# Optimization experiments

Hardware: AMD Instinct MI355X
Metric: run time of the kernel (lower is better)

Reference implementation:

```python
import jax, jax.numpy as jnp
import numpy as np

N, E, H, D, IN = 50000, 800000, 4, 64, 2  # nodes, edges, heads, head_dim, in_dim
NEG_SLOPE = 0.2  # DGL GATConv default leaky_relu slope


def setup_inputs() -> dict:
    key = jax.random.key(0)
    ks = jax.random.split(key, 16)
    p = lambda k, shape: jax.random.normal(k, shape, jnp.float32) * 0.1
    return dict(
        positions=jax.random.normal(ks[0], (N, IN), jnp.float32),
        src=jax.random.randint(ks[1], (E,), 0, N, jnp.int32),
        dst=jax.random.randint(ks[2], (E,), 0, N, jnp.int32),
        # conv1: in=2 -> 4 heads x 64; residual needs a projection (2 != 256)
        W1=p(ks[3], (IN, H * D)), al1=p(ks[4], (H, D)), ar1=p(ks[5], (H, D)),
        resW1=p(ks[6], (IN, H * D)),
        # conv2/conv3: in=256 == H*D -> identity residual in DGL
        W2=p(ks[7], (H * D, H * D)), al2=p(ks[8], (H, D)), ar2=p(ks[9], (H, D)),
        W3=p(ks[10], (H * D, H * D)), al3=p(ks[11], (H, D)), ar3=p(ks[12], (H, D)),
        # edge-scoring MLP: Linear(64,64)+ReLU, Linear(64,1)+Sigmoid
        mW1=p(ks[13], (D, D)), mb1=jnp.zeros((D,), jnp.float32),
        mW2=p(ks[14], (D, 1)), mb2=jnp.zeros((1,), jnp.float32),
    )


def _gat_layer(h, W, al, ar, src, dst, res, activation):
    """One DGL-style GATConv. h:[N,Fin] -> [N,H,D]. res:[N,H,D] residual."""
    feat = (h @ W).reshape(N, H, D)
    el = (feat * al).sum(-1)                       # [N,H]
    er = (feat * ar).sum(-1)                       # [N,H]
    e = jax.nn.leaky_relu(el[src] + er[dst], NEG_SLOPE)  # [E,H]
    # edge softmax over incoming edges of each dst node
    emax = jax.ops.segment_max(e, dst, num_segments=N)
    emax = jnp.where(jnp.isfinite(emax), emax, 0.0)      # guard empty segments
    ex = jnp.exp(e - emax[dst])
    den = jax.ops.segment_sum(ex, dst, num_segments=N)
    alpha = ex / jnp.maximum(den, 1e-9)[dst]             # [E,H]
    out = jax.ops.segment_sum(feat[src] * alpha[:, :, None], dst, num_segments=N)
    out = out + res
    if activation:
        out = jax.nn.relu(out)
    return out


def reference(positions, W1, al1, ar1, resW1, W2, al2, ar2, W3, al3, ar3,
              mW1, mb1, mW2, mb2, src, dst):
    res1 = (positions @ resW1).reshape(N, H, D)
    h = _gat_layer(positions, W1, al1, ar1, src, dst, res1, True).reshape(N, H * D)
    h = _gat_layer(h, W2, al2, ar2, src, dst, h.reshape(N, H, D), True).reshape(N, H * D)
    h = _gat_layer(h, W3, al3, ar3, src, dst, h.reshape(N, H, D), False).mean(1)  # [N,D]
    x = jnp.abs(h[src] - h[dst])                   # [E,D]
    score = jax.nn.sigmoid(jax.nn.relu(x @ mW1 + mb1) @ mW2 + mb2)
    return score.squeeze(-1)                       # [E]
```

## Files before the change

kernel.cpp:

```cpp
#include <hip/hip_runtime.h>
#include <hip/hip_bf16.h>

#define NN 50000
#define EE 800000

typedef short short8 __attribute__((ext_vector_type(8)));
typedef float f32x4 __attribute__((ext_vector_type(4)));

__device__ __forceinline__ float lrelu(float x) { return x > 0.f ? x : 0.2f * x; }

__device__ __forceinline__ unsigned short f2bf(float x) {
    __hip_bfloat16 b = __float2bfloat16(x);
    return *(unsigned short*)&b;
}
__device__ __forceinline__ float bf2f(unsigned short u) {
    return __uint_as_float(((unsigned int)u) << 16);
}

__global__ void hist_k(const int* __restrict__ dst, int* __restrict__ deg) {
    int i = blockIdx.x * 256 + threadIdx.x;
    if (i < EE) atomicAdd(&deg[dst[i]], 1);
}

__global__ __launch_bounds__(1024) void scan_k(const int* __restrict__ deg,
                                               int* __restrict__ row_ptr,
                                               int* __restrict__ cursor) {
    __shared__ int wsum[16];
    int tid = threadIdx.x, lane = tid & 63, w = tid >> 6;
    int carry = 0;
    for (int base = 0; base < NN; base += 1024) {
        int i = base + tid;
        int v = (i < NN) ? deg[i] : 0;
        int x = v;
#pragma unroll
        for (int off = 1; off < 64; off <<= 1) {
            int y = __shfl_up(x, off);
            if (lane >= off) x += y;
        }
        if (lane == 63) wsum[w] = x;
        __syncthreads();
        if (tid < 16) {
            int s = wsum[tid];
#pragma unroll
            for (int off = 1; off < 16; off <<= 1) {
                int y = __shfl_up(s, off);
                if (tid >= off) s += y;
            }
            wsum[tid] = s;
        }
        __syncthreads();
        int woff = w ? wsum[w - 1] : 0;
        int excl = carry + woff + x - v;
        if (i < NN) { row_ptr[i] = excl; cursor[i] = excl; }
        carry += wsum[15];
        __syncthreads();
    }
    if (tid == 0) row_ptr[NN] = carry;
}

__global__ void scatter_k(const int* __restrict__ src, const int* __restrict__ dst,
                          int* __restrict__ cursor, int* __restrict__ csr_src) {
    int i = blockIdx.x * 256 + threadIdx.x;
    if (i < EE) {
        int slot = atomicAdd(&cursor[dst[i]], 1);
        csr_src[slot] = src[i];
    }
}

__global__ __launch_bounds__(256) void bconv_k(const float* __restrict__ W2,
                                               const float* __restrict__ W3,
                                               const float* __restrict__ mW1,
                                               unsigned short* __restrict__ BT2,
                                               unsigned short* __restrict__ BT3,
                                               unsigned short* __restrict__ W1Tb) {
    int tid = blockIdx.x * 256 + threadIdx.x;
    int k = tid & 255, n = tid >> 8;
    BT2[n * 256 + k] = f2bf(W2[k * 256 + n]);
    BT3[n * 256 + k] = f2bf(W3[k * 256 + n]);
    if (tid < 4096) {
        int kk = tid & 63, nn = tid >> 6;
        W1Tb[nn * 64 + kk] = f2bf(mW1[kk * 64 + nn]);
    }
}

__global__ __launch_bounds__(256) void eler1_k(const float* __restrict__ pos,
                                               const float* __restrict__ W1,
                                               const float* __restrict__ al,
                                               const float* __restrict__ ar,
                                               float* __restrict__ el,
                                               float* __restrict__ er) {
    int wid = blockIdx.x * 4 + (threadIdx.x >> 6);
    int lane = threadIdx.x & 63;
    if (wid >= NN) return;
    int f = lane * 4;
    float4 w0 = *(const float4*)&W1[f];
    float4 w1 = *(const float4*)&W1[256 + f];
    float4 a4 = *(const float4*)&al[f];
    float4 r4 = *(const float4*)&ar[f];
    float2 p = *(const float2*)&pos[wid * 2];
    float fx = p.x * w0.x + p.y * w1.x;
    float fy = p.x * w0.y + p.y * w1.y;
    float fz = p.x * w0.z + p.y * w1.z;
    float fw = p.x * w0.w + p.y * w1.w;
    float pl = fx * a4.x + fy * a4.y + fz * a4.z + fw * a4.w;
    float pr = fx * r4.x + fy * r4.y + fz * r4.z + fw * r4.w;
#pragma unroll
    for (int off = 1; off < 16; off <<= 1) {
        pl += __shfl_xor(pl, off);
        pr += __shfl_xor(pr, off);
    }
    if ((lane & 15) == 0) {
        int h = lane >> 4;
        el[wid * 4 + h] = pl;
        er[wid * 4 + h] = pr;
    }
}

__global__ __launch_bounds__(256) void eler_b_k(const unsigned short* __restrict__ featb,
                                                const float* __restrict__ al,
                                                const float* __restrict__ ar,
                                                float* __restrict__ el,
                                                float* __restrict__ er) {
    int wid = blockIdx.x * 4 + (threadIdx.x >> 6);
    int lane = threadIdx.x & 63;
    if (wid >= NN) return;
    int f = lane * 4;
    ushort4 u = *(const ushort4*)&featb[(size_t)wid * 256 + f];
    float4 a4 = *(const float4*)&al[f];
    float4 r4 = *(const float4*)&ar[f];
    float vx = bf2f(u.x), vy = bf2f(u.y), vz = bf2f(u.z), vw = bf2f(u.w);
    float pl = vx * a4.x + vy * a4.y + vz * a4.z + vw * a4.w;
    float pr = vx * r4.x + vy * r4.y + vz * r4.z + vw * r4.w;
#pragma unroll
    for (int off = 1; off < 16; off <<= 1) {
        pl += __shfl_xor(pl, off);
        pr += __shfl_xor(pr, off);
    }
    if ((lane & 15) == 0) {
        int h = lane >> 4;
        el[wid * 4 + h] = pl;
        er[wid * 4 + h] = pr;
    }
}

__global__ __launch_bounds__(256) void agg1_k(const float* __restrict__ pos,
                                              const float* __restrict__ W1,
                                              const float* __restrict__ resW1,
                                              const float* __restrict__ el,
                                              const float* __restrict__ er,
                                              const int* __restrict__ row_ptr,
                                              const int* __restrict__ csr_src,
                                              float* __restrict__ hout,
                                              unsigned short* __restrict__ hb16) {
    int wid = blockIdx.x * 4 + (threadIdx.x >> 6);
    int lane = threadIdx.x & 63;
    if (wid >= NN) return;
    int f = lane * 4;
    int start = row_ptr[wid], end = row_ptr[wid + 1];
    int h = lane >> 4;
    float eh = er[wid * 4 + h];

    float ap0 = 0.f, ap1 = 0.f, den = 0.f;
    int s = start;
    for (; s + 3 < end; s += 4) {
        int sn0 = csr_src[s], sn1 = csr_src[s + 1];
        int sn2 = csr_src[s + 2], sn3 = csr_src[s + 3];
        float e0 = el[sn0 * 4 + h], e1 = el[sn1 * 4 + h];
        float e2 = el[sn2 * 4 + h], e3 = el[sn3 * 4 + h];
        float2 p0 = *(const float2*)&pos[sn0 * 2];
        float2 p1 = *(const float2*)&pos[sn1 * 2];
        float2 p2 = *(const float2*)&pos[sn2 * 2];
        float2 p3 = *(const float2*)&pos[sn3 * 2];
        float w0 = __expf(lrelu(e0 + eh)), w1 = __expf(lrelu(e1 + eh));
        float w2 = __expf(lrelu(e2 + eh)), w3 = __expf(lrelu(e3 + eh));
        den += (w0 + w1) + (w2 + w3);
        ap0 += w0 * p0.x + w1 * p1.x + w2 * p2.x + w3 * p3.x;
        ap1 += w0 * p0.y + w1 * p1.y + w2 * p2.y + w3 * p3.y;
    }
    for (; s < end; ++s) {
        int sn = csr_src[s];
        float w = __expf(lrelu(el[sn * 4 + h] + eh));
        float2 p = *(const float2*)&pos[sn * 2];
        den += w;
        ap0 += w * p.x;
        ap1 += w * p.y;
    }
    float inv = 1.f / fmaxf(den, 1e-9f);
    ap0 *= inv;
    ap1 *= inv;

    float4 w0 = *(const float4*)&W1[f];
    float4 w1 = *(const float4*)&W1[256 + f];
    float4 rw0 = *(const float4*)&resW1[f];
    float4 rw1 = *(const float4*)&resW1[256 + f];
    float2 pd = *(const float2*)&pos[wid * 2];
    float4 o;
    o.x = fmaxf(ap0 * w0.x + ap1 * w1.x + pd.x * rw0.x + pd.y * rw1.x, 0.f);
    o.y = fmaxf(ap0 * w0.y + ap1 * w1.y + pd.x * rw0.y + pd.y * rw1.y, 0.f);
    o.z = fmaxf(ap0 * w0.z + ap1 * w1.z + pd.x * rw0.z + pd.y * rw1.z, 0.f);
    o.w = fmaxf(ap0 * w0.w + ap1 * w1.w + pd.x * rw0.w + pd.y * rw1.w, 0.f);
    *(float4*)&hout[(size_t)wid * 256 + f] = o;
    ushort4 ob;
    ob.x = f2bf(o.x); ob.y = f2bf(o.y); ob.z = f2bf(o.z); ob.w = f2bf(o.w);
    *(ushort4*)&hb16[(size_t)wid * 256 + f] = ob;
}

__global__ __launch_bounds__(256) void agg_k(const unsigned short* __restrict__ featb,
                                             const float* __restrict__ el,
                                             const float* __restrict__ er,
                                             const int* __restrict__ row_ptr,
                                             const int* __restrict__ csr_src,
                                             float* __restrict__ hio,
                                             unsigned short* __restrict__ hb16) {
    int wid = blockIdx.x * 4 + (threadIdx.x >> 6);
    int lane = threadIdx.x & 63;
    if (wid >= NN) return;
    int f = lane * 4;
    int start = row_ptr[wid], end = row_ptr[wid + 1];
    int h = lane >> 4;
    float eh = er[wid * 4 + h];

    float4 acc = {0.f, 0.f, 0.f, 0.f};
    float den = 0.f;
    int s = start;
    for (; s + 3 < end; s += 4) {
        int sn0 = csr_src[s], sn1 = csr_src[s + 1];
        int sn2 = csr_src[s + 2], sn3 = csr_src[s + 3];
        float e0 = el[sn0 * 4 + h], e1 = el[sn1 * 4 + h];
        float e2 = el[sn2 * 4 + h], e3 = el[sn3 * 4 + h];
        ushort4 v0 = *(const ushort4*)&featb[(size_t)sn0 * 256 + f];
        ushort4 v1 = *(const ushort4*)&featb[(size_t)sn1 * 256 + f];
        ushort4 v2 = *(const ushort4*)&featb[(size_t)sn2 * 256 + f];
        ushort4 v3 = *(const ushort4*)&featb[(size_t)sn3 * 256 + f];
        float w0 = __expf(lrelu(e0 + eh)), w1 = __expf(lrelu(e1 + eh));
        float w2 = __expf(lrelu(e2 + eh)), w3 = __expf(lrelu(e3 + eh));
        den += (w0 + w1) + (w2 + w3);
        acc.x += w0 * bf2f(v0.x) + w1 * bf2f(v1.x) + w2 * bf2f(v2.x) + w3 * bf2f(v3.x);
        acc.y += w0 * bf2f(v0.y) + w1 * bf2f(v1.y) + w2 * bf2f(v2.y) + w3 * bf2f(v3.y);
        acc.z += w0 * bf2f(v0.z) + w1 * bf2f(v1.z) + w2 * bf2f(v2.z) + w3 * bf2f(v3.z);
        acc.w += w0 * bf2f(v0.w) + w1 * bf2f(v1.w) + w2 * bf2f(v2.w) + w3 * bf2f(v3.w);
    }
    for (; s < end; ++s) {
        int sn = csr_src[s];
        float w = __expf(lrelu(el[sn * 4 + h] + eh));
        ushort4 v = *(const ushort4*)&featb[(size_t)sn * 256 + f];
        den += w;
        acc.x += w * bf2f(v.x);
        acc.y += w * bf2f(v.y);
        acc.z += w * bf2f(v.z);
        acc.w += w * bf2f(v.w);
    }
    float inv = 1.f / fmaxf(den, 1e-9f);
    float4 r = *(const float4*)&hio[(size_t)wid * 256 + f];
    float4 o;
    o.x = fmaxf(acc.x * inv + r.x, 0.f);
    o.y = fmaxf(acc.y * inv + r.y, 0.f);
    o.z = fmaxf(acc.z * inv + r.z, 0.f);
    o.w = fmaxf(acc.w * inv + r.w, 0.f);
    *(float4*)&hio[(size_t)wid * 256 + f] = o;
    ushort4 ob;
    ob.x = f2bf(o.x); ob.y = f2bf(o.y); ob.z = f2bf(o.z); ob.w = f2bf(o.w);
    *(ushort4*)&hb16[(size_t)wid * 256 + f] = ob;
}

__global__ __launch_bounds__(256) void agg3_k(const unsigned short* __restrict__ featb,
                                              const float* __restrict__ el,
                                              const float* __restrict__ er,
                                              const int* __restrict__ row_ptr,
                                              const int* __restrict__ csr_src,
                                              const float* __restrict__ hres,
                                              unsigned short* __restrict__ hsmallb) {
    int wid = blockIdx.x * 4 + (threadIdx.x >> 6);
    int lane = threadIdx.x & 63;
    if (wid >= NN) return;
    int f = lane * 4;
    int start = row_ptr[wid], end = row_ptr[wid + 1];
    int h = lane >> 4;
    float eh = er[wid * 4 + h];

    float4 acc = {0.f, 0.f, 0.f, 0.f};
    float den = 0.f;
    int s = start;
    for (; s + 3 < end; s += 4) {
        int sn0 = csr_src[s], sn1 = csr_src[s + 1];
        int sn2 = csr_src[s + 2], sn3 = csr_src[s + 3];
        float e0 = el[sn0 * 4 + h], e1 = el[sn1 * 4 + h];
        float e2 = el[sn2 * 4 + h], e3 = el[sn3 * 4 + h];
        ushort4 v0 = *(const ushort4*)&featb[(size_t)sn0 * 256 + f];
        ushort4 v1 = *(const ushort4*)&featb[(size_t)sn1 * 256 + f];
        ushort4 v2 = *(const ushort4*)&featb[(size_t)sn2 * 256 + f];
        ushort4 v3 = *(const ushort4*)&featb[(size_t)sn3 * 256 + f];
        float w0 = __expf(lrelu(e0 + eh)), w1 = __expf(lrelu(e1 + eh));
        float w2 = __expf(lrelu(e2 + eh)), w3 = __expf(lrelu(e3 + eh));
        den += (w0 + w1) + (w2 + w3);
        acc.x += w0 * bf2f(v0.x) + w1 * bf2f(v1.x) + w2 * bf2f(v2.x) + w3 * bf2f(v3.x);
        acc.y += w0 * bf2f(v0.y) + w1 * bf2f(v1.y) + w2 * bf2f(v2.y) + w3 * bf2f(v3.y);
        acc.z += w0 * bf2f(v0.z) + w1 * bf2f(v1.z) + w2 * bf2f(v2.z) + w3 * bf2f(v3.z);
        acc.w += w0 * bf2f(v0.w) + w1 * bf2f(v1.w) + w2 * bf2f(v2.w) + w3 * bf2f(v3.w);
    }
    for (; s < end; ++s) {
        int sn = csr_src[s];
        float w = __expf(lrelu(el[sn * 4 + h] + eh));
        ushort4 v = *(const ushort4*)&featb[(size_t)sn * 256 + f];
        den += w;
        acc.x += w * bf2f(v.x);
        acc.y += w * bf2f(v.y);
        acc.z += w * bf2f(v.z);
        acc.w += w * bf2f(v.w);
    }
    float inv = 1.f / fmaxf(den, 1e-9f);
    float4 r = *(const float4*)&hres[(size_t)wid * 256 + f];
    float4 o;
    o.x = acc.x * inv + r.x;
    o.y = acc.y * inv + r.y;
    o.z = acc.z * inv + r.z;
    o.w = acc.w * inv + r.w;
    o.x += __shfl_xor(o.x, 16); o.y += __shfl_xor(o.y, 16);
    o.z += __shfl_xor(o.z, 16); o.w += __shfl_xor(o.w, 16);
    o.x += __shfl_xor(o.x, 32); o.y += __shfl_xor(o.y, 32);
    o.z += __shfl_xor(o.z, 32); o.w += __shfl_xor(o.w, 32);
    if (lane < 16) {
        ushort4 m4;
        m4.x = f2bf(o.x * 0.25f);
        m4.y = f2bf(o.y * 0.25f);
        m4.z = f2bf(o.z * 0.25f);
        m4.w = f2bf(o.w * 0.25f);
        *(ushort4*)&hsmallb[(size_t)wid * 64 + lane * 4] = m4;
    }
}

__global__ __launch_bounds__(256) void gemm_mfma_k(const unsigned short* __restrict__ Ab,
                                                   const unsigned short* __restrict__ BT,
                                                   unsigned short* __restrict__ C) {
    __shared__ __align__(16) short As[128 * 40];
    __shared__ __align__(16) short Bs[128 * 40];
    int tid = threadIdx.x;
    int lane = tid & 63, wave = tid >> 6;
    int wr = wave >> 1, wc = wave & 1;
    int tileM = blockIdx.x * 128;
    int tileN = blockIdx.y * 128;

    int srow = tid >> 1, sko = (tid & 1) * 16;
    int fm = lane & 15, kg = lane >> 4;

    f32x4 acc[4][4];
#pragma unroll
    for (int i = 0; i < 4; ++i)
#pragma unroll
        for (int j = 0; j < 4; ++j) acc[i][j] = (f32x4){0.f, 0.f, 0.f, 0.f};

    for (int k0 = 0; k0 < 256; k0 += 32) {
        int gr = tileM + srow;
        short8 a0 = (short8)0, a1 = (short8)0;
        if (gr < NN) {
            a0 = *(const short8*)&Ab[(size_t)gr * 256 + k0 + sko];
            a1 = *(const short8*)&Ab[(size_t)gr * 256 + k0 + sko + 8];
        }
        *(short8*)&As[srow * 40 + sko] = a0;
        *(short8*)&As[srow * 40 + sko + 8] = a1;
        short8 b0 = *(const short8*)&BT[(size_t)(tileN + srow) * 256 + k0 + sko];
        short8 b1 = *(const short8*)&BT[(size_t)(tileN + srow) * 256 + k0 + sko + 8];
        *(short8*)&Bs[srow * 40 + sko] = b0;
        *(short8*)&Bs[srow * 40 + sko + 8] = b1;
        __syncthreads();

        short8 afr[4], bfr[4];
#pragma unroll
        for (int mi = 0; mi < 4; ++mi)
            afr[mi] = *(const short8*)&As[(wr * 64 + mi * 16 + fm) * 40 + kg * 8];
#pragma unroll
        for (int ni = 0; ni < 4; ++ni)
            bfr[ni] = *(const short8*)&Bs[(wc * 64 + ni * 16 + fm) * 40 + kg * 8];
#pragma unroll
        for (int mi = 0; mi < 4; ++mi)
#pragma unroll
            for (int ni = 0; ni < 4; ++ni)
                acc[mi][ni] = __builtin_amdgcn_mfma_f32_16x16x32_bf16(
                    afr[mi], bfr[ni], acc[mi][ni], 0, 0, 0);
        __syncthreads();
    }

#pragma unroll
    for (int mi = 0; mi < 4; ++mi) {
#pragma unroll
        for (int ni = 0; ni < 4; ++ni) {
            int col = tileN + wc * 64 + ni * 16 + fm;
#pragma unroll
            for (int r = 0; r < 4; ++r) {
                int row = tileM + wr * 64 + mi * 16 + kg * 4 + r;
                if (row < NN) C[(size_t)row * 256 + col] = f2bf(acc[mi][ni][r]);
            }
        }
    }
}

__global__ __launch_bounds__(256) void edge_score4_k(const unsigned short* __restrict__ hs,
                                                     const int* __restrict__ src,
                                                     const int* __restrict__ dst,
                                                     const unsigned short* __restrict__ W1Tb,
                                                     const float* __restrict__ mb1,
                                                     const float* __restrict__ mW2,
                                                     const float* __restrict__ mb2,
                                                     float* __restrict__ out) {
    __shared__ __align__(16) unsigned short xs[64 * 72];
    __shared__ __align__(16) unsigned short wt[64 * 72];
    __shared__ float b1s[64], w2s[64];
    int tid = threadIdx.x;
    int e_loc = tid >> 2, q = tid & 3;

    *(short8*)&wt[e_loc * 72 + q * 16]     = *(const short8*)&W1Tb[e_loc * 64 + q * 16];
    *(short8*)&wt[e_loc * 72 + q * 16 + 8] = *(const short8*)&W1Tb[e_loc * 64 + q * 16 + 8];
    if (tid < 64) { b1s[tid] = mb1[tid]; w2s[tid] = mW2[tid]; }

    int e = blockIdx.x * 64 + e_loc;
    int s = src[e], d = dst[e];
    const unsigned short* rs = &hs[(size_t)s * 64 + q * 16];
    const unsigned short* rd = &hs[(size_t)d * 64 + q * 16];
    short8 a0 = *(const short8*)&rs[0];
    short8 a1 = *(const short8*)&rs[8];
    short8 b0 = *(const short8*)&rd[0];
    short8 b1 = *(const short8*)&rd[8];
    short8 x0, x1;
#pragma unroll
    for (int i = 0; i < 8; ++i) {
        x0[i] = (short)f2bf(fabsf(bf2f((unsigned short)a0[i]) - bf2f((unsigned short)b0[i])));
        x1[i] = (short)f2bf(fabsf(bf2f((unsigned short)a1[i]) - bf2f((unsigned short)b1[i])));
    }
    *(short8*)&xs[e_loc * 72 + q * 16]     = x0;
    *(short8*)&xs[e_loc * 72 + q * 16 + 8] = x1;
    __syncthreads();

    int lane = tid & 63, w = tid >> 6;
    int fm = lane & 15, kg = lane >> 4;

    const unsigned short* arow = &xs[(w * 16 + fm) * 72];
    short8 af0 = *(const short8*)&arow[kg * 8];
    short8 af1 = *(const short8*)&arow[32 + kg * 8];

    f32x4 acc[4];
#pragma unroll
    for (int ni = 0; ni < 4; ++ni) acc[ni] = (f32x4){0.f, 0.f, 0.f, 0.f};
#pragma unroll
    for (int ni = 0; ni < 4; ++ni) {
        const unsigned short* brow = &wt[(ni * 16 + fm) * 72];
        short8 bf0 = *(const short8*)&brow[kg * 8];
        short8 bf1 = *(const short8*)&brow[32 + kg * 8];
        acc[ni] = __builtin_amdgcn_mfma_f32_16x16x32_bf16(af0, bf0, acc[ni], 0, 0, 0);
        acc[ni] = __builtin_amdgcn_mfma_f32_16x16x32_bf16(af1, bf1, acc[ni], 0, 0, 0);
    }

    float t0 = 0.f, t1 = 0.f, t2 = 0.f, t3 = 0.f;
#pragma unroll
    for (int ni = 0; ni < 4; ++ni) {
        int n = ni * 16 + fm;
        float bb = b1s[n], ww = w2s[n];
        t0 += fmaxf(acc[ni][0] + bb, 0.f) * ww;
        t1 += fmaxf(acc[ni][1] + bb, 0.f) * ww;
        t2 += fmaxf(acc[ni][2] + bb, 0.f) * ww;
        t3 += fmaxf(acc[ni][3] + bb, 0.f) * ww;
    }
#pragma unroll
    for (int off = 1; off < 16; off <<= 1) {
        t0 += __shfl_xor(t0, off);
        t1 += __shfl_xor(t1, off);
        t2 += __shfl_xor(t2, off);
        t3 += __shfl_xor(t3, off);
    }
    if (fm == 0) {
        float bias = mb2[0];
        int base = blockIdx.x * 64 + w * 16 + kg * 4;
        out[base + 0] = 1.f / (1.f + __expf(-(t0 + bias)));
        out[base + 1] = 1.f / (1.f + __expf(-(t1 + bias)));
        out[base + 2] = 1.f / (1.f + __expf(-(t2 + bias)));
        out[base + 3] = 1.f / (1.f + __expf(-(t3 + bias)));
    }
}

extern "C" void kernel_launch(void* const* d_in, const int* in_sizes, int n_in,
                              void* d_out, int out_size, void* d_ws, size_t ws_size,
                              hipStream_t stream) {
    (void)in_sizes; (void)n_in; (void)out_size; (void)ws_size;
    const float* pos   = (const float*)d_in[0];
    const int*   src   = (const int*)d_in[1];
    const int*   dst   = (const int*)d_in[2];
    const float* W1    = (const float*)d_in[3];
    const float* al1   = (const float*)d_in[4];
    const float* ar1   = (const float*)d_in[5];
    const float* resW1 = (const float*)d_in[6];
    const float* W2    = (const float*)d_in[7];
    const float* al2   = (const float*)d_in[8];
    const float* ar2   = (const float*)d_in[9];
    const float* W3    = (const float*)d_in[10];
    const float* al3   = (const float*)d_in[11];
    const float* ar3   = (const float*)d_in[12];
    const float* mW1   = (const float*)d_in[13];
    const float* mb1   = (const float*)d_in[14];
    const float* mW2   = (const float*)d_in[15];
    const float* mb2   = (const float*)d_in[16];
    float* out = (float*)d_out;

    char* ws = (char*)d_ws;
    size_t off = 0;
    auto alloc = [&](size_t bytes) {
        void* p = ws + off;
        off += (bytes + 255) & ~(size_t)255;
        return p;
    };
    float* Hbuf            = (float*)alloc((size_t)NN * 256 * 4);
    unsigned short* FEATb  = (unsigned short*)alloc((size_t)NN * 256 * 2);
    unsigned short* Hb16   = (unsigned short*)alloc((size_t)NN * 256 * 2);
    unsigned short* BT2    = (unsigned short*)alloc((size_t)256 * 256 * 2);
    unsigned short* BT3    = (unsigned short*)alloc((size_t)256 * 256 * 2);
    unsigned short* W1Tb   = (unsigned short*)alloc((size_t)64 * 64 * 2);
    unsigned short* hsmallb = (unsigned short*)alloc((size_t)NN * 64 * 2);
    float* el     = (float*)alloc((size_t)NN * 4 * 4);
    float* er     = (float*)alloc((size_t)NN * 4 * 4);
    int* deg      = (int*)alloc((size_t)NN * 4);
    int* row_ptr  = (int*)alloc((size_t)(NN + 1) * 4);
    int* cursor   = (int*)alloc((size_t)NN * 4);
    int* csr      = (int*)alloc((size_t)EE * 4);

    hipMemsetAsync(deg, 0, (size_t)NN * 4, stream);
    hist_k<<<(EE + 255) / 256, 256, 0, stream>>>(dst, deg);
    scan_k<<<1, 1024, 0, stream>>>(deg, row_ptr, cursor);
    scatter_k<<<(EE + 255) / 256, 256, 0, stream>>>(src, dst, cursor, csr);
    bconv_k<<<256, 256, 0, stream>>>(W2, W3, mW1, BT2, BT3, W1Tb);

    eler1_k<<<NN / 4 + 1, 256, 0, stream>>>(pos, W1, al1, ar1, el, er);
    agg1_k<<<NN / 4 + 1, 256, 0, stream>>>(pos, W1, resW1, el, er, row_ptr, csr, Hbuf, Hb16);

    dim3 ggrid((NN + 127) / 128, 2);
    gemm_mfma_k<<<ggrid, 256, 0, stream>>>(Hb16, BT2, FEATb);
    eler_b_k<<<NN / 4 + 1, 256, 0, stream>>>(FEATb, al2, ar2, el, er);
    agg_k<<<NN / 4 + 1, 256, 0, stream>>>(FEATb, el, er, row_ptr, csr, Hbuf, Hb16);

    gemm_mfma_k<<<ggrid, 256, 0, stream>>>(Hb16, BT3, FEATb);
    eler_b_k<<<NN / 4 + 1, 256, 0, stream>>>(FEATb, al3, ar3, el, er);
    agg3_k<<<NN / 4 + 1, 256, 0, stream>>>(FEATb, el, er, row_ptr, csr, Hbuf, hsmallb);

    edge_score4_k<<<EE / 64, 256, 0, stream>>>(hsmallb, src, dst, W1Tb, mb1, mW2, mb2, out);
}
```

Measured before the change: 506.0 us.

## Fuse el/er projection into GEMM epilogue and drop fp32 residual buffer

The attention logits el/er are now computed in the MFMA GEMM epilogue from the fp32 accumulators, so the separate eler_b_k kernels, with their launch and reread of the feature matrix, go away. The fp32 hidden-state buffer is also removed; residuals are read from the bf16 copy, cutting the fp32 write and read per layer. This computes logits from unrounded fp32 values and adds residuals from bf16, which changes numerics slightly. It also adds shuffle work and register pressure to the GEMM.

Result: faster. 494.0 us (-2.4%).

```diff
diff --git a/kernel.cpp b/kernel.cpp
--- a/kernel.cpp
+++ b/kernel.cpp
@@ -116,33 +116,6 @@
     }
 }
 
-__global__ __launch_bounds__(256) void eler_b_k(const unsigned short* __restrict__ featb,
-                                                const float* __restrict__ al,
-                                                const float* __restrict__ ar,
-                                                float* __restrict__ el,
-                                                float* __restrict__ er) {
-    int wid = blockIdx.x * 4 + (threadIdx.x >> 6);
-    int lane = threadIdx.x & 63;
-    if (wid >= NN) return;
-    int f = lane * 4;
-    ushort4 u = *(const ushort4*)&featb[(size_t)wid * 256 + f];
-    float4 a4 = *(const float4*)&al[f];
-    float4 r4 = *(const float4*)&ar[f];
-    float vx = bf2f(u.x), vy = bf2f(u.y), vz = bf2f(u.z), vw = bf2f(u.w);
-    float pl = vx * a4.x + vy * a4.y + vz * a4.z + vw * a4.w;
-    float pr = vx * r4.x + vy * r4.y + vz * r4.z + vw * r4.w;
-#pragma unroll
-    for (int off = 1; off < 16; off <<= 1) {
-        pl += __shfl_xor(pl, off);
-        pr += __shfl_xor(pr, off);
-    }
-    if ((lane & 15) == 0) {
-        int h = lane >> 4;
-        el[wid * 4 + h] = pl;
-        er[wid * 4 + h] = pr;
-    }
-}
-
 __global__ __launch_bounds__(256) void agg1_k(const float* __restrict__ pos,
                                               const float* __restrict__ W1,
                                               const float* __restrict__ resW1,
@@ -150,7 +123,6 @@
                                               const float* __restrict__ er,
                                               const int* __restrict__ row_ptr,
                                               const int* __restrict__ csr_src,
-                                              float* __restrict__ hout,
                                               unsigned short* __restrict__ hb16) {
     int wid = blockIdx.x * 4 + (threadIdx.x >> 6);
     int lane = threadIdx.x & 63;
@@ -199,7 +171,6 @@
     o.y = fmaxf(ap0 * w0.y + ap1 * w1.y + pd.x * rw0.y + pd.y * rw1.y, 0.f);
     o.z = fmaxf(ap0 * w0.z + ap1 * w1.z + pd.x * rw0.z + pd.y * rw1.z, 0.f);
     o.w = fmaxf(ap0 * w0.w + ap1 * w1.w + pd.x * rw0.w + pd.y * rw1.w, 0.f);
-    *(float4*)&hout[(size_t)wid * 256 + f] = o;
     ushort4 ob;
     ob.x = f2bf(o.x); ob.y = f2bf(o.y); ob.z = f2bf(o.z); ob.w = f2bf(o.w);
     *(ushort4*)&hb16[(size_t)wid * 256 + f] = ob;
@@ -210,7 +181,6 @@
                                              const float* __restrict__ er,
                                              const int* __restrict__ row_ptr,
                                              const int* __restrict__ csr_src,
-                                             float* __restrict__ hio,
                                              unsigned short* __restrict__ hb16) {
     int wid = blockIdx.x * 4 + (threadIdx.x >> 6);
     int lane = threadIdx.x & 63;
@@ -251,13 +221,12 @@
         acc.w += w * bf2f(v.w);
     }
     float inv = 1.f / fmaxf(den, 1e-9f);
-    float4 r = *(const float4*)&hio[(size_t)wid * 256 + f];
+    ushort4 rb = *(const ushort4*)&hb16[(size_t)wid * 256 + f];
     float4 o;
-    o.x = fmaxf(acc.x * inv + r.x, 0.f);
-    o.y = fmaxf(acc.y * inv + r.y, 0.f);
-    o.z = fmaxf(acc.z * inv + r.z, 0.f);
-    o.w = fmaxf(acc.w * inv + r.w, 0.f);
-    *(float4*)&hio[(size_t)wid * 256 + f] = o;
+    o.x = fmaxf(acc.x * inv + bf2f(rb.x), 0.f);
+    o.y = fmaxf(acc.y * inv + bf2f(rb.y), 0.f);
+    o.z = fmaxf(acc.z * inv + bf2f(rb.z), 0.f);
+    o.w = fmaxf(acc.w * inv + bf2f(rb.w), 0.f);
     ushort4 ob;
     ob.x = f2bf(o.x); ob.y = f2bf(o.y); ob.z = f2bf(o.z); ob.w = f2bf(o.w);
     *(ushort4*)&hb16[(size_t)wid * 256 + f] = ob;
@@ -268,7 +237,7 @@
                                               const float* __restrict__ er,
                                               const int* __restrict__ row_ptr,
                                               const int* __restrict__ csr_src,
-                                              const float* __restrict__ hres,
+                                              const unsigned short* __restrict__ hresb,
                                               unsigned short* __restrict__ hsmallb) {
     int wid = blockIdx.x * 4 + (threadIdx.x >> 6);
     int lane = threadIdx.x & 63;
@@ -309,12 +278,12 @@
         acc.w += w * bf2f(v.w);
     }
     float inv = 1.f / fmaxf(den, 1e-9f);
-    float4 r = *(const float4*)&hres[(size_t)wid * 256 + f];
+    ushort4 rb = *(const ushort4*)&hresb[(size_t)wid * 256 + f];
     float4 o;
-    o.x = acc.x * inv + r.x;
-    o.y = acc.y * inv + r.y;
-    o.z = acc.z * inv + r.z;
-    o.w = acc.w * inv + r.w;
+    o.x = acc.x * inv + bf2f(rb.x);
+    o.y = acc.y * inv + bf2f(rb.y);
+    o.z = acc.z * inv + bf2f(rb.z);
+    o.w = acc.w * inv + bf2f(rb.w);
     o.x += __shfl_xor(o.x, 16); o.y += __shfl_xor(o.y, 16);
     o.z += __shfl_xor(o.z, 16); o.w += __shfl_xor(o.w, 16);
     o.x += __shfl_xor(o.x, 32); o.y += __shfl_xor(o.y, 32);
@@ -331,7 +300,11 @@
 
 __global__ __launch_bounds__(256) void gemm_mfma_k(const unsigned short* __restrict__ Ab,
                                                    const unsigned short* __restrict__ BT,
-                                                   unsigned short* __restrict__ C) {
+                                                   const float* __restrict__ al,
+                                                   const float* __restrict__ ar,
+                                                   unsigned short* __restrict__ C,
+                                                   float* __restrict__ el,
+                                                   float* __restrict__ er) {
     __shared__ __align__(16) short As[128 * 40];
     __shared__ __align__(16) short Bs[128 * 40];
     int tid = threadIdx.x;
@@ -389,6 +362,36 @@
             for (int r = 0; r < 4; ++r) {
                 int row = tileM + wr * 64 + mi * 16 + kg * 4 + r;
                 if (row < NN) C[(size_t)row * 256 + col] = f2bf(acc[mi][ni][r]);
+            }
+        }
+    }
+
+    int h = blockIdx.y * 2 + wc;
+    float al_r[4], ar_r[4];
+#pragma unroll
+    for (int ni = 0; ni < 4; ++ni) {
+        al_r[ni] = al[h * 64 + ni * 16 + fm];
+        ar_r[ni] = ar[h * 64 + ni * 16 + fm];
+    }
+#pragma unroll
+    for (int mi = 0; mi < 4; ++mi) {
+#pragma unroll
+        for (int r = 0; r < 4; ++r) {
+            float tl = acc[mi][0][r] * al_r[0] + acc[mi][1][r] * al_r[1] +
+                       acc[mi][2][r] * al_r[2] + acc[mi][3][r] * al_r[3];
+            float tr = acc[mi][0][r] * ar_r[0] + acc[mi][1][r] * ar_r[1] +
+                       acc[mi][2][r] * ar_r[2] + acc[mi][3][r] * ar_r[3];
+#pragma unroll
+            for (int off = 1; off < 16; off <<= 1) {
+                tl += __shfl_xor(tl, off);
+                tr += __shfl_xor(tr, off);
+            }
+            if (fm == 0) {
+                int row = tileM + wr * 64 + mi * 16 + kg * 4 + r;
+                if (row < NN) {
+                    el[row * 4 + h] = tl;
+                    er[row * 4 + h] = tr;
+                }
             }
         }
     }
@@ -506,7 +509,6 @@
         off += (bytes + 255) & ~(size_t)255;
         return p;
     };
-    float* Hbuf            = (float*)alloc((size_t)NN * 256 * 4);
     unsigned short* FEATb  = (unsigned short*)alloc((size_t)NN * 256 * 2);
     unsigned short* Hb16   = (unsigned short*)alloc((size_t)NN * 256 * 2);
     unsigned short* BT2    = (unsigned short*)alloc((size_t)256 * 256 * 2);
@@ -527,16 +529,14 @@
     bconv_k<<<256, 256, 0, stream>>>(W2, W3, mW1, BT2, BT3, W1Tb);
 
     eler1_k<<<NN / 4 + 1, 256, 0, stream>>>(pos, W1, al1, ar1, el, er);
-    agg1_k<<<NN / 4 + 1, 256, 0, stream>>>(pos, W1, resW1, el, er, row_ptr, csr, Hbuf, Hb16);
+    agg1_k<<<NN / 4 + 1, 256, 0, stream>>>(pos, W1, resW1, el, er, row_ptr, csr, Hb16);
 
     dim3 ggrid((NN + 127) / 128, 2);
-    gemm_mfma_k<<<ggrid, 256, 0, stream>>>(Hb16, BT2, FEATb);
-    eler_b_k<<<NN / 4 + 1, 256, 0, stream>>>(FEATb, al2, ar2, el, er);
-    agg_k<<<NN / 4 + 1, 256, 0, stream>>>(FEATb, el, er, row_ptr, csr, Hbuf, Hb16);
-
-    gemm_mfma_k<<<ggrid, 256, 0, stream>>>(Hb16, BT3, FEATb);
-    eler_b_k<<<NN / 4 + 1, 256, 0, stream>>>(FEATb, al3, ar3, el, er);
-    agg3_k<<<NN / 4 + 1, 256, 0, stream>>>(FEATb, el, er, row_ptr, csr, Hbuf, hsmallb);
+    gemm_mfma_k<<<ggrid, 256, 0, stream>>>(Hb16, BT2, al2, ar2, FEATb, el, er);
+    agg_k<<<NN / 4 + 1, 256, 0, stream>>>(FEATb, el, er, row_ptr, csr, Hb16);
+
+    gemm_mfma_k<<<ggrid, 256, 0, stream>>>(Hb16, BT3, al3, ar3, FEATb, el, er);
+    agg3_k<<<NN / 4 + 1, 256, 0, stream>>>(FEATb, el, er, row_ptr, csr, Hb16, hsmallb);
 
     edge_score4_k<<<EE / 64, 256, 0, stream>>>(hsmallb, src, dst, W1Tb, mb1, mW2, mb2, out);
 }
```
